# Kernel tuning notes

Measured on AMD Instinct MI355X. Metric: run time of the kernel, lower is better.

## Reference

```python
import jax, jax.numpy as jnp
import numpy as np

# Config constants matching init_kwargs (layer_no=2 -> stride 8, anch_mask=[0,1,2])
ANCHORS = np.array([[10,13],[16,30],[33,23],[30,61],[62,45],[59,119],
                    [116,90],[156,198],[373,326]], np.float32)
STRIDE = 8.0
N_CLASSES = 80
A = 3          # n_anchors in this head
IGNORE = 0.7   # ignore_thre
LAMBDA = 0.5


def _forward(xin, labels, W, b):
    B = xin.shape[0]
    F = xin.shape[2]
    n_ch = 5 + N_CLASSES
    anchors = jnp.asarray(ANCHORS) / STRIDE      # all_anchors_grid, [9,2]
    m_anch = anchors[:A]                         # masked_anchors (anch_mask=[0,1,2])

    # 1x1 conv -> [B, A, F, F, n_ch]
    out = jnp.einsum('bchw,oc->bohw', xin, W) + b[None, :, None, None]
    out = out.reshape(B, A, n_ch, F, F).transpose(0, 1, 3, 4, 2)
    ch = jnp.arange(n_ch)
    output = jnp.where((ch < 2) | (ch >= 4), jax.nn.sigmoid(out), out)

    # box decode (pred); only [..., :4] is used (detached) for IoU ignore mask
    xs = jnp.arange(F, dtype=xin.dtype)
    pred_x = output[..., 0] + xs                 # x varies along last spatial axis
    pred_y = output[..., 1] + xs[:, None]        # y varies along rows
    pred_w = jnp.exp(output[..., 2]) * m_anch[:, 0][None, :, None, None]
    pred_h = jnp.exp(output[..., 3]) * m_anch[:, 1][None, :, None, None]
    pred4 = jax.lax.stop_gradient(jnp.stack([pred_x, pred_y, pred_w, pred_h], -1))

    lab = jax.lax.stop_gradient(labels)          # original uses labels.cpu().data
    valid = lab.sum(-1) > 0                      # [B,K]
    tx = lab[..., 1] * F
    ty = lab[..., 2] * F
    tw = lab[..., 3] * F
    th = lab[..., 4] * F
    ti = tx.astype(jnp.int32)
    tj = ty.astype(jnp.int32)
    tbox = jnp.stack([tx, ty, tw, th], -1)       # [B,K,4]

    # anchor matching: bboxes_iou(truth_box, ref_anchors) with xyxy=True, faithful to source
    ref = jnp.concatenate([jnp.zeros_like(anchors), anchors], -1)   # [9,4] = [0,0,w,h]
    tl = jnp.maximum(tbox[..., None, :2], ref[:, :2])
    br = jnp.minimum(tbox[..., None, 2:], ref[:, 2:])
    area_a = jnp.prod(tbox[..., 2:] - tbox[..., :2], -1)            # [B,K]
    area_b = anchors[:, 0] * anchors[:, 1]                          # [9]
    ai = jnp.prod(br - tl, -1) * jnp.all(tl < br, -1)
    a_iou = ai / (area_a[..., None] + area_b - ai)                  # [B,K,9]
    a_iou = jnp.where(valid[..., None], a_iou, -1.0)
    best_all = jnp.argmax(a_iou, -1)                                # [B,K]
    best_mask = best_all < A                                        # in anch_mask {0,1,2}
    best_n = best_all % A

    # pred-vs-truth IoU (xywh) -> objectness ignore mask
    p = pred4.reshape(B, -1, 4)                                     # [B, A*F*F, 4]
    ptl = p[..., :2] - p[..., 2:] * 0.5
    pbr = p[..., :2] + p[..., 2:] * 0.5
    ttl = tbox[..., :2] - tbox[..., 2:] * 0.5
    tbr = tbox[..., :2] + tbox[..., 2:] * 0.5
    tl2 = jnp.maximum(ptl[:, :, None], ttl[:, None])                # [B,N,K,2]
    br2 = jnp.minimum(pbr[:, :, None], tbr[:, None])
    ai2 = jnp.prod(br2 - tl2, -1) * jnp.all(tl2 < br2, -1)
    denom = (p[..., 2] * p[..., 3])[:, :, None] + (tbox[..., 2] * tbox[..., 3])[:, None, :] - ai2
    piou = jnp.where(valid[:, None, :], ai2 / denom, 0.0)
    obj_mask = 1.0 - (piou.max(-1) > IGNORE).astype(xin.dtype).reshape(B, A, F, F)

    # vectorized scatter of per-truth-box assignments
    assign = valid & best_mask
    bidx = jnp.broadcast_to(jnp.arange(B)[:, None], valid.shape)
    lin = ((bidx * A + best_n) * F + tj) * F + ti
    ncells = B * A * F * F
    lin = jnp.where(assign, lin, ncells).reshape(-1)    # OOB rows dropped in scatter

    aw = m_anch[best_n, 0]
    ah = m_anch[best_n, 1]
    onehot = jax.nn.one_hot(lab[..., 0].astype(jnp.int32), N_CLASSES, dtype=xin.dtype)
    tvec = jnp.concatenate([
        (tx - ti)[..., None], (ty - tj)[..., None],
        jnp.log(tw / aw + 1e-16)[..., None], jnp.log(th / ah + 1e-16)[..., None],
        jnp.ones_like(tx)[..., None], onehot], -1).reshape(-1, n_ch)
    scale = jnp.sqrt(2.0 - tw * th / (F * F))           # [B,K]

    obj_mask = obj_mask.reshape(-1).at[lin].set(1.0, mode='drop').reshape(B, A, F, F)
    tgt_mask = jnp.zeros((ncells, 4 + N_CLASSES), xin.dtype).at[lin].set(1.0, mode='drop')
    tgt_mask = tgt_mask.reshape(B, A, F, F, 4 + N_CLASSES)
    tgt_scale = jnp.zeros((ncells, 2), xin.dtype).at[lin].set(
        jnp.stack([scale, scale], -1).reshape(-1, 2), mode='drop').reshape(B, A, F, F, 2)
    target = jnp.zeros((ncells, n_ch), xin.dtype).at[lin].set(tvec, mode='drop')
    target = target.reshape(B, A, F, F, n_ch)

    def process(x):
        xy = x[..., :2] * tgt_mask[..., :2]
        wh = x[..., 2:4] * tgt_mask[..., 2:4] * tgt_scale
        obj = (x[..., 4] * obj_mask)[..., None]
        cl = x[..., 5:] * tgt_mask[..., 4:]
        return jnp.concatenate([xy, wh, obj, cl], -1)

    o = process(output)
    t = process(target)

    def bce(p_, t_, w=None):
        # torch BCELoss clamps log terms at -100
        l = -(t_ * jnp.maximum(jnp.log(p_), -100.0)
              + (1.0 - t_) * jnp.maximum(jnp.log(1.0 - p_), -100.0))
        return (l * w if w is not None else l).sum()

    loss_xy = bce(o[..., :2], t[..., :2], tgt_scale * tgt_scale)
    loss_wh = LAMBDA * ((o[..., 2:4] - t[..., 2:4]) ** 2).sum()
    loss_obj = bce(o[..., 4], t[..., 4])
    loss_cls = bce(o[..., 5:], t[..., 5:])
    loss_l2 = ((o - t) ** 2).sum()
    loss = loss_xy + loss_wh + loss_obj + loss_cls
    return jnp.stack([loss, loss_xy, loss_wh, loss_obj, loss_cls, loss_l2])


def setup_inputs() -> dict:
    key = jax.random.key(0)
    k1, k2, k3, k4, k5 = jax.random.split(key, 5)
    B, C, F, K = 16, 256, 76, 40
    n_ch = 5 + N_CLASSES
    xin = jax.random.normal(k1, (B, C, F, F), jnp.float32)
    W = jax.random.normal(k2, (A * n_ch, C), jnp.float32) * 0.02  # 1x1 conv weight
    b = jnp.zeros((A * n_ch,), jnp.float32)
    cls = jax.random.randint(k3, (B, K, 1), 0, N_CLASSES).astype(jnp.float32)
    xy = jax.random.uniform(k4, (B, K, 2), jnp.float32, 0.05, 0.95)
    wh = jax.random.uniform(k5, (B, K, 2), jnp.float32, 0.02, 0.4)
    labels = jnp.concatenate([cls, xy, wh], -1)   # [B,K,5] = [class,xc,yc,w,h]
    return {"xin": xin, "labels": labels, "W": W, "b": b}


def reference(xin, labels, W, b):
    return _forward(xin, labels, W, b)
```

## Files before the change

### kernel.cpp

```cpp
#include <hip/hip_runtime.h>
#include <math.h>

typedef unsigned int u32;
typedef unsigned short u16;
typedef __attribute__((ext_vector_type(4))) u32 u32x4;
typedef __attribute__((ext_vector_type(8))) short bf16x8;
typedef __attribute__((ext_vector_type(4))) float f32x4;

#define FDIM 76
#define NCELL 5776
#define NA 3
#define NCH 85
#define NCLS 80
#define KLAB 40
#define NB 16
#define CIN 256
#define TILES_PER_B 91
#define NBLK (NB * TILES_PER_B)
#define CS_LD 68

typedef __attribute__((address_space(1))) const void gvoid_t;
typedef __attribute__((address_space(3))) void svoid_t;

__device__ __forceinline__ float sigmf_(float x) { return __frcp_rn(1.0f + __expf(-x)); }
__device__ __forceinline__ float bce_fullf(float p, float t) {
    return -(t * fmaxf(__logf(p), -100.0f) + (1.0f - t) * fmaxf(__logf(1.0f - p), -100.0f));
}
__device__ __forceinline__ float bce1f(float p) { return -fmaxf(__logf(p), -100.0f); }
__device__ __forceinline__ float bce0f(float p) { return -fmaxf(__logf(1.0f - p), -100.0f); }

__device__ __forceinline__ u16 bf16rne(float f) {
    u32 u = __float_as_uint(f);
    u32 r = u + 0x7fffu + ((u >> 16) & 1u);
    return (u16)(r >> 16);
}
__device__ __forceinline__ float bf16f(u16 v) { return __uint_as_float(((u32)v) << 16); }

__global__ __launch_bounds__(256) void yolo_prep(const float* __restrict__ W,
                                                 const float* __restrict__ labels,
                                                 u16* __restrict__ Wbf,
                                                 float* __restrict__ lrec) {
    if (blockIdx.x < 256) {
        int idx = blockIdx.x * 256 + threadIdx.x;
        int row = idx >> 8, col = idx & 255;
        float v = (row < NA * NCH) ? W[row * CIN + col] : 0.0f;
        Wbf[idx] = bf16rne(v);
        return;
    }
    for (int idx = threadIdx.x; idx < NB * KLAB; idx += 256) {
        const float* l = labels + idx * 5;
        float cls = l[0], x = l[1], y = l[2], ww = l[3], hh = l[4];
        bool valid = (cls + x + y + ww + hh) > 0.0f;
        float tx = x * FDIM, ty = y * FDIM, tw = ww * FDIM, th = hh * FDIM;
        int ti = (int)tx, tj = (int)ty;
        float area_a = (tw - tx) * (th - ty);
        const float aw[9] = {1.25f, 2.0f, 4.125f, 3.75f, 7.75f, 7.375f, 14.5f, 19.5f, 46.625f};
        const float ah[9] = {1.625f, 3.75f, 2.875f, 7.625f, 5.625f, 14.875f, 11.25f, 24.75f, 40.75f};
        float best = -1e30f;
        int bi = 0;
        for (int n = 0; n < 9; n++) {
            float bw = fminf(tw, aw[n]), bh = fminf(th, ah[n]);
            float ai = ((tx < bw) && (ty < bh)) ? (bw - tx) * (bh - ty) : 0.0f;
            float iou = valid ? ai / (area_a + aw[n] * ah[n] - ai) : -1.0f;
            if (iou > best) { best = iou; bi = n; }
        }
        int bn = bi % 3;
        bool assign = valid && (bi < 3);
        float* r = lrec + idx * 16;
        r[0] = tx - 0.5f * tw; r[1] = ty - 0.5f * th;
        r[2] = tx + 0.5f * tw; r[3] = ty + 0.5f * th;
        r[4] = tw * th;
        r[5] = valid ? 1.0f : 0.0f;
        r[6] = assign ? (float)((bn * FDIM + tj) * FDIM + ti) : -1.0f;
        r[7] = sqrtf(2.0f - tw * th / (float)(FDIM * FDIM));
        r[8] = tx - (float)ti; r[9] = ty - (float)tj;
        r[10] = logf(tw / aw[bn] + 1e-16f); r[11] = logf(th / ah[bn] + 1e-16f);
        r[12] = cls; r[13] = 0.0f; r[14] = 0.0f; r[15] = 0.0f;
    }
}

__global__ __launch_bounds__(512, 6) void yolo_mfma(const float* __restrict__ xin,
                                                    const u16* __restrict__ Wbf,
                                                    const float* __restrict__ bias,
                                                    const float* __restrict__ lrec,
                                                    float* __restrict__ partials) {
    __shared__ char smem[40960];
    float* S0  = (float*)smem;
    float* S1  = (float*)(smem + 16384);
    u16*   A   = (u16*)(smem + 32768);
    u16*   Csb = (u16*)smem;
    float* red = (float*)(smem + 40704);

    const int blk = blockIdx.x;
    const int b = blk / TILES_PER_B;
    const int tile = blk - b * TILES_PER_B;
    const int cell0 = tile * 64;
    const int t = threadIdx.x;
    const int lane = t & 63;
    const int wid = t >> 6;
    const int g = lane >> 4;
    const int l15 = lane & 15;

    const float* xbase = xin + (size_t)b * CIN * NCELL;
    const float* lb = lrec + b * KLAB * 16;
    const int cg0 = cell0 + lane;
    const int cg = cg0 < NCELL ? cg0 : NCELL - 1;

#pragma unroll
    for (int i = 0; i < 8; i++) {
        const int kl = wid * 8 + i;
        __builtin_amdgcn_global_load_lds(
            (gvoid_t*)(xbase + (size_t)kl * NCELL + cg),
            (svoid_t*)(S0 + kl * 64), 4, 0, 0);
    }

    f32x4 acc[2][4];
#pragma unroll
    for (int mi = 0; mi < 2; mi++)
#pragma unroll
        for (int ni = 0; ni < 4; ni++) acc[mi][ni] = (f32x4){0.f, 0.f, 0.f, 0.f};

    const u16* wrow = Wbf + (wid * 32 + l15) * CIN;

#pragma unroll
    for (int c = 0; c < 4; c++) {
        float* Sc = (c & 1) ? S1 : S0;
        bf16x8 af[4];
#pragma unroll
        for (int s2 = 0; s2 < 2; s2++)
#pragma unroll
            for (int mi = 0; mi < 2; mi++)
                af[s2 * 2 + mi] = *(const bf16x8*)(wrow + mi * 16 * CIN + c * 64 + s2 * 32 + g * 8);
        if (c < 3) {
            float* Sn = (c & 1) ? S0 : S1;
#pragma unroll
            for (int i = 0; i < 8; i++) {
                const int kl = wid * 8 + i;
                __builtin_amdgcn_global_load_lds(
                    (gvoid_t*)(xbase + (size_t)((c + 1) * 64 + kl) * NCELL + cg),
                    (svoid_t*)(Sn + kl * 64), 4, 0, 0);
            }
            asm volatile("s_waitcnt vmcnt(8) lgkmcnt(0)" ::: "memory");
        } else {
            asm volatile("s_waitcnt vmcnt(0) lgkmcnt(0)" ::: "memory");
        }
        __builtin_amdgcn_sched_barrier(0);
        __builtin_amdgcn_s_barrier();
        __builtin_amdgcn_sched_barrier(0);
        {
            const float* sp = Sc + wid * 8 * 64 + lane;
            u32x4 v;
#pragma unroll
            for (int e = 0; e < 4; e++) {
                float f0 = sp[(2 * e) * 64];
                float f1 = sp[(2 * e + 1) * 64];
                v[e] = (u32)bf16rne(f0) | ((u32)bf16rne(f1) << 16);
            }
            const int byte = (lane * 128 + wid * 16) ^ ((lane & 7) << 4);
            *(u32x4*)((char*)A + byte) = v;
        }
        asm volatile("s_waitcnt lgkmcnt(0)" ::: "memory");
        __builtin_amdgcn_sched_barrier(0);
        __builtin_amdgcn_s_barrier();
        __builtin_amdgcn_sched_barrier(0);
#pragma unroll
        for (int s2 = 0; s2 < 2; s2++) {
#pragma unroll
            for (int ni = 0; ni < 4; ni++) {
                const int cell = ni * 16 + l15;
                const int byte = (cell * 128 + s2 * 64 + g * 16) ^ ((cell & 7) << 4);
                bf16x8 bfr = *(const bf16x8*)((char*)A + byte);
                acc[0][ni] = __builtin_amdgcn_mfma_f32_16x16x32_bf16(af[s2 * 2 + 0], bfr, acc[0][ni], 0, 0, 0);
                acc[1][ni] = __builtin_amdgcn_mfma_f32_16x16x32_bf16(af[s2 * 2 + 1], bfr, acc[1][ni], 0, 0, 0);
            }
        }
    }

    __syncthreads();

    float bv[8];
#pragma unroll
    for (int mi = 0; mi < 2; mi++)
#pragma unroll
        for (int reg = 0; reg < 4; reg++) {
            const int ch = wid * 32 + mi * 16 + g * 4 + reg;
            bv[mi * 4 + reg] = (ch < NA * NCH) ? bias[ch] : 0.0f;
        }
#pragma unroll
    for (int mi = 0; mi < 2; mi++)
#pragma unroll
        for (int ni = 0; ni < 4; ni++)
#pragma unroll
            for (int reg = 0; reg < 4; reg++) {
                const int ch = wid * 32 + mi * 16 + g * 4 + reg;
                const int cell = ni * 16 + l15;
                Csb[ch * CS_LD + cell] = bf16rne(acc[mi][ni][reg] + bv[mi * 4 + reg]);
            }
    __syncthreads();

    float part[5] = {0.f, 0.f, 0.f, 0.f, 0.f};
    if (t < 384) {
        const int half = (t >= 192) ? 1 : 0;
        const int unit = t - half * 192;
        const int a = unit >> 6;
        const int c = unit & 63;
        const int cgl = cell0 + c;
        if (cgl < NCELL) {
            const int chb = a * NCH;
            const int hh = cgl / FDIM;
            const int ww = cgl - hh * FDIM;
            const float mykey = (float)((a * FDIM + hh) * FDIM + ww);
            if (half == 0) {
                float v0 = bf16f(Csb[(chb + 0) * CS_LD + c]);
                float v1 = bf16f(Csb[(chb + 1) * CS_LD + c]);
                float v2 = bf16f(Csb[(chb + 2) * CS_LD + c]);
                float v3 = bf16f(Csb[(chb + 3) * CS_LD + c]);
                float v4 = bf16f(Csb[(chb + 4) * CS_LD + c]);
                const float manw[3] = {1.25f, 2.0f, 4.125f};
                const float manh[3] = {1.625f, 3.75f, 2.875f};
                float s0 = sigmf_(v0), s1 = sigmf_(v1), s4 = sigmf_(v4);
                float pw = __expf(v2) * manw[a];
                float ph = __expf(v3) * manh[a];
                float px = s0 + (float)ww, py = s1 + (float)hh;
                float parea = pw * ph;
                float ptlx = px - 0.5f * pw, ptly = py - 0.5f * ph;
                float pbrx = px + 0.5f * pw, pbry = py + 0.5f * ph;
                float maxiou = -1e30f;
                int aidx = -1;
                for (int k = 0; k < KLAB; k++) {
                    const f32x4 Aq = *(const f32x4*)(lb + k * 16);
                    const f32x4 Bq = *(const f32x4*)(lb + k * 16 + 4);
                    float tlx = fmaxf(ptlx, Aq.x), tly = fmaxf(ptly, Aq.y);
                    float brx = fminf(pbrx, Aq.z), bry = fminf(pbry, Aq.w);
                    float inter = ((tlx < brx) && (tly < bry)) ? (brx - tlx) * (bry - tly) : 0.0f;
                    float iou = (Bq.y != 0.0f) ? inter * __frcp_rn(parea + Bq.x - inter) : 0.0f;
                    maxiou = fmaxf(maxiou, iou);
                    if (Bq.z == mykey) aidx = k;
                }
                if (aidx >= 0) {
                    const f32x4 Bq = *(const f32x4*)(lb + aidx * 16 + 4);
                    const f32x4 Tv = *(const f32x4*)(lb + aidx * 16 + 8);
                    float sc = Bq.w, sc2 = sc * sc;
                    part[0] += sc2 * (bce_fullf(s0, Tv.x) + bce_fullf(s1, Tv.y));
                    float dw = v2 - Tv.z, dh = v3 - Tv.w;
                    float whq = dw * dw + dh * dh;
                    part[1] += 0.5f * sc2 * whq;
                    part[2] += bce1f(s4);
                    int ci = (int)lb[aidx * 16 + 12];
                    float l2 = (s0 - Tv.x) * (s0 - Tv.x) + (s1 - Tv.y) * (s1 - Tv.y) +
                               sc2 * whq + (s4 - 1.0f) * (s4 - 1.0f);
                    float lcls = 0.0f;
                    for (int cc = 0; cc < 40; cc++) {
                        float s = sigmf_(bf16f(Csb[(chb + 5 + cc) * CS_LD + c]));
                        if (cc == ci) { lcls += bce1f(s); l2 += (s - 1.0f) * (s - 1.0f); }
                        else          { lcls += bce0f(s); l2 += s * s; }
                    }
                    part[3] += lcls; part[4] += l2;
                } else {
                    bool objm = !(maxiou > 0.7f);
                    if (objm) { part[2] += bce0f(s4); part[4] += s4 * s4; }
                }
            } else {
                int aidx = -1;
                for (int k = 0; k < KLAB; k++) {
                    if (lb[k * 16 + 6] == mykey) aidx = k;
                }
                if (aidx >= 0) {
                    int ci = (int)lb[aidx * 16 + 12];
                    float lcls = 0.0f, l2 = 0.0f;
                    for (int cc = 40; cc < 80; cc++) {
                        float s = sigmf_(bf16f(Csb[(chb + 5 + cc) * CS_LD + c]));
                        if (cc == ci) { lcls += bce1f(s); l2 += (s - 1.0f) * (s - 1.0f); }
                        else          { lcls += bce0f(s); l2 += s * s; }
                    }
                    part[3] += lcls; part[4] += l2;
                }
            }
        }
    }

#pragma unroll
    for (int i = 0; i < 5; i++) {
        float v = part[i];
        for (int off = 32; off > 0; off >>= 1) v += __shfl_down(v, off);
        if ((t & 63) == 0) red[(t >> 6) * 8 + i] = v;
    }
    __syncthreads();
    if (t == 0) {
#pragma unroll
        for (int i = 0; i < 5; i++) {
            float s = red[i];
#pragma unroll
            for (int wv = 1; wv < 8; wv++) s += red[wv * 8 + i];
            partials[blk * 8 + i] = s;
        }
    }
}

__global__ __launch_bounds__(256) void yolo_fin(const float* __restrict__ partials,
                                                float* __restrict__ out, int n) {
    __shared__ float red[4][8];
    const int t = threadIdx.x;
    float s[5] = {0.f, 0.f, 0.f, 0.f, 0.f};
    for (int r = t; r < n; r += 256)
#pragma unroll
        for (int i = 0; i < 5; i++) s[i] += partials[r * 8 + i];
#pragma unroll
    for (int i = 0; i < 5; i++) {
        float v = s[i];
        for (int off = 32; off > 0; off >>= 1) v += __shfl_down(v, off);
        if ((t & 63) == 0) red[t >> 6][i] = v;
    }
    __syncthreads();
    if (t == 0) {
        float xy  = red[0][0] + red[1][0] + red[2][0] + red[3][0];
        float wh  = red[0][1] + red[1][1] + red[2][1] + red[3][1];
        float obj = red[0][2] + red[1][2] + red[2][2] + red[3][2];
        float cls = red[0][3] + red[1][3] + red[2][3] + red[3][3];
        float l2  = red[0][4] + red[1][4] + red[2][4] + red[3][4];
        out[0] = xy + wh + obj + cls;
        out[1] = xy; out[2] = wh; out[3] = obj; out[4] = cls; out[5] = l2;
    }
}

extern "C" void kernel_launch(void* const* d_in, const int* in_sizes, int n_in,
                              void* d_out, int out_size, void* d_ws, size_t ws_size,
                              hipStream_t stream) {
    const float* xin    = (const float*)d_in[0];
    const float* labels = (const float*)d_in[1];
    const float* Wm     = (const float*)d_in[2];
    const float* bias   = (const float*)d_in[3];
    float* out = (float*)d_out;

    float* partials = (float*)d_ws;
    float* lrec  = (float*)((char*)d_ws + 46592);
    u16*   Wbf   = (u16*)((char*)d_ws + 46592 + 40960);

    yolo_prep<<<257, 256, 0, stream>>>(Wm, labels, Wbf, lrec);
    yolo_mfma<<<NBLK, 512, 0, stream>>>(xin, Wbf, bias, lrec, partials);
    yolo_fin<<<1, 256, 0, stream>>>(partials, out, NBLK);
}
```

Baseline: 70.97 us.

## Use 16-byte LDS-direct loads and split label IoU scan across thread halves

The input staging switches from per-lane 4-byte global_load_lds to 16-byte loads, with each lane fetching four consecutive cells of one channel row. This cuts load instruction count and the vmcnt wait depth. The 40-label IoU/assignment scan is now split 20/20 between the two thread halves, and the partial max-IoU and match index are merged through shared memory. This costs an extra barrier but halves the serial label loop that the first half previously ran alone.

```diff
diff --git a/kernel.cpp b/kernel.cpp
--- a/kernel.cpp
+++ b/kernel.cpp
@@ -89,6 +89,7 @@
     float* S1  = (float*)(smem + 16384);
     u16*   A   = (u16*)(smem + 32768);
     u16*   Csb = (u16*)smem;
+    float* mrg = (float*)(smem + 34816);
     float* red = (float*)(smem + 40704);
 
     const int blk = blockIdx.x;
@@ -103,15 +104,18 @@
 
     const float* xbase = xin + (size_t)b * CIN * NCELL;
     const float* lb = lrec + b * KLAB * 16;
-    const int cg0 = cell0 + lane;
-    const int cg = cg0 < NCELL ? cg0 : NCELL - 1;
-
-#pragma unroll
-    for (int i = 0; i < 8; i++) {
-        const int kl = wid * 8 + i;
+
+    const int q = lane >> 4;
+    const int r4 = (lane & 15) * 4;
+    int cq = cell0 + r4;
+    if (cq > NCELL - 4) cq = NCELL - 4;
+
+#pragma unroll
+    for (int i = 0; i < 2; i++) {
+        const int k0 = wid * 8 + i * 4;
         __builtin_amdgcn_global_load_lds(
-            (gvoid_t*)(xbase + (size_t)kl * NCELL + cg),
-            (svoid_t*)(S0 + kl * 64), 4, 0, 0);
+            (gvoid_t*)(xbase + (size_t)(k0 + q) * NCELL + cq),
+            (svoid_t*)(S0 + k0 * 64), 16, 0, 0);
     }
 
     f32x4 acc[2][4];
@@ -134,13 +138,13 @@
         if (c < 3) {
             float* Sn = (c & 1) ? S0 : S1;
 #pragma unroll
-            for (int i = 0; i < 8; i++) {
-                const int kl = wid * 8 + i;
+            for (int i = 0; i < 2; i++) {
+                const int k0 = wid * 8 + i * 4;
                 __builtin_amdgcn_global_load_lds(
-                    (gvoid_t*)(xbase + (size_t)((c + 1) * 64 + kl) * NCELL + cg),
-                    (svoid_t*)(Sn + kl * 64), 4, 0, 0);
-            }
-            asm volatile("s_waitcnt vmcnt(8) lgkmcnt(0)" ::: "memory");
+                    (gvoid_t*)(xbase + (size_t)((c + 1) * 64 + k0 + q) * NCELL + cq),
+                    (svoid_t*)(Sn + k0 * 64), 16, 0, 0);
+            }
+            asm volatile("s_waitcnt vmcnt(2) lgkmcnt(0)" ::: "memory");
         } else {
             asm volatile("s_waitcnt vmcnt(0) lgkmcnt(0)" ::: "memory");
         }
@@ -199,82 +203,97 @@
     __syncthreads();
 
     float part[5] = {0.f, 0.f, 0.f, 0.f, 0.f};
+    const int half = (t >= 192) ? 1 : 0;
+    const int unit = t - half * 192;
+    bool active = false;
+    float v0 = 0.f, v1 = 0.f, v2 = 0.f, v3 = 0.f, v4 = 0.f;
+    float s0 = 0.f, s1 = 0.f, s4 = 0.f;
+    float mIoU = -1e30f;
+    int aidxp = -1;
+    int a = 0, cc_ = 0, hh = 0, ww = 0, chb = 0;
+    float mykey = 0.f;
+
     if (t < 384) {
-        const int half = (t >= 192) ? 1 : 0;
-        const int unit = t - half * 192;
-        const int a = unit >> 6;
-        const int c = unit & 63;
-        const int cgl = cell0 + c;
+        a = unit >> 6;
+        cc_ = unit & 63;
+        const int cgl = cell0 + cc_;
         if (cgl < NCELL) {
-            const int chb = a * NCH;
-            const int hh = cgl / FDIM;
-            const int ww = cgl - hh * FDIM;
-            const float mykey = (float)((a * FDIM + hh) * FDIM + ww);
-            if (half == 0) {
-                float v0 = bf16f(Csb[(chb + 0) * CS_LD + c]);
-                float v1 = bf16f(Csb[(chb + 1) * CS_LD + c]);
-                float v2 = bf16f(Csb[(chb + 2) * CS_LD + c]);
-                float v3 = bf16f(Csb[(chb + 3) * CS_LD + c]);
-                float v4 = bf16f(Csb[(chb + 4) * CS_LD + c]);
-                const float manw[3] = {1.25f, 2.0f, 4.125f};
-                const float manh[3] = {1.625f, 3.75f, 2.875f};
-                float s0 = sigmf_(v0), s1 = sigmf_(v1), s4 = sigmf_(v4);
-                float pw = __expf(v2) * manw[a];
-                float ph = __expf(v3) * manh[a];
-                float px = s0 + (float)ww, py = s1 + (float)hh;
-                float parea = pw * ph;
-                float ptlx = px - 0.5f * pw, ptly = py - 0.5f * ph;
-                float pbrx = px + 0.5f * pw, pbry = py + 0.5f * ph;
-                float maxiou = -1e30f;
-                int aidx = -1;
-                for (int k = 0; k < KLAB; k++) {
-                    const f32x4 Aq = *(const f32x4*)(lb + k * 16);
-                    const f32x4 Bq = *(const f32x4*)(lb + k * 16 + 4);
-                    float tlx = fmaxf(ptlx, Aq.x), tly = fmaxf(ptly, Aq.y);
-                    float brx = fminf(pbrx, Aq.z), bry = fminf(pbry, Aq.w);
-                    float inter = ((tlx < brx) && (tly < bry)) ? (brx - tlx) * (bry - tly) : 0.0f;
-                    float iou = (Bq.y != 0.0f) ? inter * __frcp_rn(parea + Bq.x - inter) : 0.0f;
-                    maxiou = fmaxf(maxiou, iou);
-                    if (Bq.z == mykey) aidx = k;
+            active = true;
+            chb = a * NCH;
+            hh = cgl / FDIM;
+            ww = cgl - hh * FDIM;
+            mykey = (float)((a * FDIM + hh) * FDIM + ww);
+            v0 = bf16f(Csb[(chb + 0) * CS_LD + cc_]);
+            v1 = bf16f(Csb[(chb + 1) * CS_LD + cc_]);
+            v2 = bf16f(Csb[(chb + 2) * CS_LD + cc_]);
+            v3 = bf16f(Csb[(chb + 3) * CS_LD + cc_]);
+            v4 = bf16f(Csb[(chb + 4) * CS_LD + cc_]);
+            const float manw[3] = {1.25f, 2.0f, 4.125f};
+            const float manh[3] = {1.625f, 3.75f, 2.875f};
+            s0 = sigmf_(v0); s1 = sigmf_(v1); s4 = sigmf_(v4);
+            float pw = __expf(v2) * manw[a];
+            float ph = __expf(v3) * manh[a];
+            float px = s0 + (float)ww, py = s1 + (float)hh;
+            float parea = pw * ph;
+            float ptlx = px - 0.5f * pw, ptly = py - 0.5f * ph;
+            float pbrx = px + 0.5f * pw, pbry = py + 0.5f * ph;
+            const float* lbh = lb + half * 20 * 16;
+            for (int k = 0; k < 20; k++) {
+                const f32x4 Aq = *(const f32x4*)(lbh + k * 16);
+                const f32x4 Bq = *(const f32x4*)(lbh + k * 16 + 4);
+                float tlx = fmaxf(ptlx, Aq.x), tly = fmaxf(ptly, Aq.y);
+                float brx = fminf(pbrx, Aq.z), bry = fminf(pbry, Aq.w);
+                float inter = ((tlx < brx) && (tly < bry)) ? (brx - tlx) * (bry - tly) : 0.0f;
+                float iou = (Bq.y != 0.0f) ? inter * __frcp_rn(parea + Bq.x - inter) : 0.0f;
+                mIoU = fmaxf(mIoU, iou);
+                if (Bq.z == mykey) aidxp = half * 20 + k;
+            }
+        }
+        mrg[(half * 192 + unit) * 2 + 0] = mIoU;
+        mrg[(half * 192 + unit) * 2 + 1] = (float)aidxp;
+    }
+    __syncthreads();
+
+    if (t < 384 && active) {
+        const float oIoU = mrg[((1 - half) * 192 + unit) * 2 + 0];
+        const int oaidx = (int)mrg[((1 - half) * 192 + unit) * 2 + 1];
+        const float maxiou = fmaxf(mIoU, oIoU);
+        const int aidx = (aidxp > oaidx) ? aidxp : oaidx;
+
+        if (half == 0) {
+            if (aidx >= 0) {
+                const f32x4 Bq = *(const f32x4*)(lb + aidx * 16 + 4);
+                const f32x4 Tv = *(const f32x4*)(lb + aidx * 16 + 8);
+                float sc = Bq.w, sc2 = sc * sc;
+                part[0] += sc2 * (bce_fullf(s0, Tv.x) + bce_fullf(s1, Tv.y));
+                float dw = v2 - Tv.z, dh = v3 - Tv.w;
+                float whq = dw * dw + dh * dh;
+                part[1] += 0.5f * sc2 * whq;
+                part[2] += bce1f(s4);
+                int ci = (int)lb[aidx * 16 + 12];
+                float l2 = (s0 - Tv.x) * (s0 - Tv.x) + (s1 - Tv.y) * (s1 - Tv.y) +
+                           sc2 * whq + (s4 - 1.0f) * (s4 - 1.0f);
+                float lcls = 0.0f;
+                for (int cc = 0; cc < 40; cc++) {
+                    float s = sigmf_(bf16f(Csb[(chb + 5 + cc) * CS_LD + cc_]));
+                    if (cc == ci) { lcls += bce1f(s); l2 += (s - 1.0f) * (s - 1.0f); }
+                    else          { lcls += bce0f(s); l2 += s * s; }
                 }
-                if (aidx >= 0) {
-                    const f32x4 Bq = *(const f32x4*)(lb + aidx * 16 + 4);
-                    const f32x4 Tv = *(const f32x4*)(lb + aidx * 16 + 8);
-                    float sc = Bq.w, sc2 = sc * sc;
-                    part[0] += sc2 * (bce_fullf(s0, Tv.x) + bce_fullf(s1, Tv.y));
-                    float dw = v2 - Tv.z, dh = v3 - Tv.w;
-                    float whq = dw * dw + dh * dh;
-                    part[1] += 0.5f * sc2 * whq;
-                    part[2] += bce1f(s4);
-                    int ci = (int)lb[aidx * 16 + 12];
-                    float l2 = (s0 - Tv.x) * (s0 - Tv.x) + (s1 - Tv.y) * (s1 - Tv.y) +
-                               sc2 * whq + (s4 - 1.0f) * (s4 - 1.0f);
-                    float lcls = 0.0f;
-                    for (int cc = 0; cc < 40; cc++) {
-                        float s = sigmf_(bf16f(Csb[(chb + 5 + cc) * CS_LD + c]));
-                        if (cc == ci) { lcls += bce1f(s); l2 += (s - 1.0f) * (s - 1.0f); }
-                        else          { lcls += bce0f(s); l2 += s * s; }
-                    }
-                    part[3] += lcls; part[4] += l2;
-                } else {
-                    bool objm = !(maxiou > 0.7f);
-                    if (objm) { part[2] += bce0f(s4); part[4] += s4 * s4; }
+                part[3] += lcls; part[4] += l2;
+            } else {
+                bool objm = !(maxiou > 0.7f);
+                if (objm) { part[2] += bce0f(s4); part[4] += s4 * s4; }
+            }
+        } else {
+            if (aidx >= 0) {
+                int ci = (int)lb[aidx * 16 + 12];
+                float lcls = 0.0f, l2 = 0.0f;
+                for (int cc = 40; cc < 80; cc++) {
+                    float s = sigmf_(bf16f(Csb[(chb + 5 + cc) * CS_LD + cc_]));
+                    if (cc == ci) { lcls += bce1f(s); l2 += (s - 1.0f) * (s - 1.0f); }
+                    else          { lcls += bce0f(s); l2 += s * s; }
                 }
-            } else {
-                int aidx = -1;
-                for (int k = 0; k < KLAB; k++) {
-                    if (lb[k * 16 + 6] == mykey) aidx = k;
-                }
-                if (aidx >= 0) {
-                    int ci = (int)lb[aidx * 16 + 12];
-                    float lcls = 0.0f, l2 = 0.0f;
-                    for (int cc = 40; cc < 80; cc++) {
-                        float s = sigmf_(bf16f(Csb[(chb + 5 + cc) * CS_LD + c]));
-                        if (cc == ci) { lcls += bce1f(s); l2 += (s - 1.0f) * (s - 1.0f); }
-                        else          { lcls += bce0f(s); l2 += s * s; }
-                    }
-                    part[3] += lcls; part[4] += l2;
-                }
+                part[3] += lcls; part[4] += l2;
             }
         }
     }
```

New measurement: 74.39 us. 1.05x slower.
